# Kernel optimization log

Measured on AMD Instinct MI355X. Metric: run time of the kernel, lower is better.

Reference implementation:

```python
import jax, jax.numpy as jnp
import numpy as np

T, B, DIM, N = 2048, 16, 1024, 64
INIT_BETA_BIAS = 2.0
EPS = 1e-6


def setup_inputs() -> dict:
    key = jax.random.key(0)
    ks = jax.random.split(key, 6)
    xavier = np.sqrt(2.0 / (N + DIM)).astype(np.float32)
    return {
        "x": jax.random.normal(ks[0], (T, B, DIM), dtype=jnp.float32),
        "S0": jnp.zeros((B, N, N), dtype=jnp.float32),
        "W_k": jax.random.normal(ks[1], (N, DIM), dtype=jnp.float32) * xavier,
        "W_v": jax.random.normal(ks[2], (N, DIM), dtype=jnp.float32) * xavier,
        "W_q": jax.random.normal(ks[3], (N, DIM), dtype=jnp.float32) * xavier,
        "W_beta": jax.random.normal(ks[4], (N, DIM), dtype=jnp.float32) * xavier,
        "b_beta": jnp.full((N,), INIT_BETA_BIAS, dtype=jnp.float32),
    }


def reference(x, S0, W_k, W_v, W_q, W_beta, b_beta):
    # Batched projections: [T, B, dim] @ [dim, n] -> [T, B, n]
    k_all = jnp.einsum("tbd,nd->tbn", x, W_k)
    v_all = jnp.einsum("tbd,nd->tbn", x, W_v)
    q_all = jnp.einsum("tbd,nd->tbn", x, W_q)
    g_all = jax.nn.sigmoid(jnp.einsum("tbd,nd->tbn", x, W_beta) + b_beta)

    def step(S, inp):
        k, v, q, g = inp  # each [B, n]
        k_norm = k / (jnp.linalg.norm(k, axis=-1, keepdims=True) + EPS)
        retrieved = jnp.einsum("bij,bj->bi", S, k_norm)
        delta = v - retrieved
        S_new = g[:, :, None] * S + delta[:, :, None] * k_norm[:, None, :]
        Sq = jnp.einsum("bij,bj->bi", S_new, q)
        out = Sq * jax.nn.silu(Sq)  # self-gated output
        return S_new, out

    S_final, output = jax.lax.scan(step, S0, (k_all, v_all, q_all, g_all))
    return output, S_final
```

## Files before the change

### kernel.cpp

```cpp
#include <hip/hip_runtime.h>
#include <math.h>

#define T_STEPS 2048
#define BATCH   16
#define DIM     1024
#define NSTATE  64
#define NFIELD  256
#define PROJ_TSTRIDE (BATCH * NFIELD)
static constexpr float EPS = 1e-6f;

#define AS1 __attribute__((address_space(1)))
#define AS3 __attribute__((address_space(3)))

typedef _Float16 f16x8 __attribute__((ext_vector_type(8)));
typedef _Float16 f16x4 __attribute__((ext_vector_type(4)));
typedef float    f32x4 __attribute__((ext_vector_type(4)));

template <int CTRL>
__device__ __forceinline__ float dpp_add(float x) {
    int yi = __builtin_amdgcn_update_dpp(0, __float_as_int(x), CTRL, 0xF, 0xF, true);
    return x + __int_as_float(yi);
}
__device__ __forceinline__ float reduce16(float x) {
    x = dpp_add<0x121>(x);
    x = dpp_add<0x122>(x);
    x = dpp_add<0x124>(x);
    x = dpp_add<0x128>(x);
    return x;
}
__device__ __forceinline__ void reduce16x2(float& x, float& y) {
    x = dpp_add<0x121>(x); y = dpp_add<0x121>(y);
    x = dpp_add<0x122>(x); y = dpp_add<0x122>(y);
    x = dpp_add<0x124>(x); y = dpp_add<0x124>(y);
    x = dpp_add<0x128>(x); y = dpp_add<0x128>(y);
}
__device__ __forceinline__ float dotp(const float4& u, const float4& w) {
    float t0 = u.x * w.x; t0 = fmaf(u.y, w.y, t0);
    float t1 = u.z * w.z; t1 = fmaf(u.w, w.w, t1);
    return t0 + t1;
}
__device__ __forceinline__ float dot4r(const float4& u, const float4& w) {
    return reduce16(dotp(u, w));
}


#define PBM   128
#define KSTEP 64
#define NKS   (DIM / KSTEP)

__global__ __launch_bounds__(256) void prep_w16(
    const float* __restrict__ Wk, const float* __restrict__ Wv,
    const float* __restrict__ Wq, const float* __restrict__ Wb,
    _Float16* __restrict__ W16)
{
    const int flat = blockIdx.x * 256 + threadIdx.x;
    const int lane = flat & 63;
    const int st   = (flat >> 6) & 31;
    const int ks   = flat >> 11;
    const int cg = st & 15, kc2 = st >> 4;
    const int col = cg * 16 + (lane & 15);
    const int field = col >> 6, wrow = col & 63;
    const float* Wf = (field == 0 ? Wk : field == 1 ? Wv : field == 2 ? Wq : Wb);
    const float* src = Wf + (size_t)wrow * DIM + ks * 64 + kc2 * 32 + (lane >> 4) * 8;
    const float4 a = *(const float4*)(src);
    const float4 b = *(const float4*)(src + 4);
    f16x8 r;
    r[0] = (_Float16)a.x; r[1] = (_Float16)a.y; r[2] = (_Float16)a.z; r[3] = (_Float16)a.w;
    r[4] = (_Float16)b.x; r[5] = (_Float16)b.y; r[6] = (_Float16)b.z; r[7] = (_Float16)b.w;
    *(f16x8*)(W16 + (size_t)flat * 8) = r;
}

__global__ __launch_bounds__(512, 1) void proj_mfma(
    const float* __restrict__ x, const _Float16* __restrict__ W16,
    const float* __restrict__ bb, float* __restrict__ proj)
{
    __shared__ _Float16 Asub[2][16][64][8];
    __shared__ _Float16 Bsub[2][32][64][8];

    const int tid = threadIdx.x;
    const int w = tid >> 6, wl = tid & 63;
    const int wm = w >> 2, wn = w & 3;
    const int l15 = wl & 15, lr = wl >> 4;
    const size_t mbase = (size_t)blockIdx.x * PBM;

    _Float16* const abase = &Asub[0][0][0][0];
    _Float16* const bbase = &Bsub[0][0][0][0];

    const float* asrc[4];
    int aoff[4];
    #pragma unroll
    for (int it = 0; it < 4; ++it) {
        const int fid = it * 512 + tid;
        const int row = fid >> 4, kq = (fid & 15) * 4;
        asrc[it] = x + (mbase + row) * (size_t)DIM + kq;
        aoff[it] = ((kq >> 5) * 8 + (row >> 4)) * 512
                 + ((row & 15) + ((kq >> 3) & 3) * 16) * 8
                 + (kq & 7);
    }
    const _Float16* bsrc[4];
    int boff[4];
    #pragma unroll
    for (int m = 0; m < 4; ++m) {
        const int st = w * 4 + m;
        bsrc[m] = W16 + ((size_t)st * 64 + wl) * 8;
        boff[m] = st * 512;
    }

    auto stageB = [&](int ks, int buf) {
        #pragma unroll
        for (int m = 0; m < 4; ++m) {
            const _Float16* g = bsrc[m] + (size_t)ks * 16384;
            void* lp = (char*)bbase + (size_t)(buf * 16384 + boff[m]) * 2;
            __builtin_amdgcn_global_load_lds((const AS1 void*)g, (AS3 void*)lp, 16, 0, 0);
        }
    };

    float4 h0[4], h1[4];
    auto loadA = [&](int ks, float4* h) {
        #pragma unroll
        for (int it = 0; it < 4; ++it)
            h[it] = *(const float4*)(asrc[it] + ks * KSTEP);
    };
    auto writeA = [&](const float4* h, int buf) {
        #pragma unroll
        for (int it = 0; it < 4; ++it) {
            f16x4 v;
            v[0] = (_Float16)h[it].x; v[1] = (_Float16)h[it].y;
            v[2] = (_Float16)h[it].z; v[3] = (_Float16)h[it].w;
            *(f16x4*)(abase + buf * 8192 + aoff[it]) = v;
        }
    };

    f32x4 acc[4][4] = {};

    loadA(0, h0);
    stageB(0, 0);
    loadA(1, h1);
    writeA(h0, 0);
    __syncthreads();

    #pragma unroll
    for (int ks = 0; ks < NKS; ++ks) {
        const int buf = ks & 1;
        if (ks + 1 < NKS) stageB(ks + 1, buf ^ 1);
        if (ks + 2 < NKS) loadA(ks + 2, (ks & 1) ? h1 : h0);

        #pragma unroll
        for (int kc = 0; kc < 2; ++kc) {
            f16x8 af[4], bf[4];
            #pragma unroll
            for (int mf = 0; mf < 4; ++mf)
                af[mf] = *(const f16x8*)&Asub[buf][kc * 8 + wm * 4 + mf][wl][0];
            #pragma unroll
            for (int nf = 0; nf < 4; ++nf)
                bf[nf] = *(const f16x8*)&Bsub[buf][kc * 16 + wn * 4 + nf][wl][0];
            #pragma unroll
            for (int mf = 0; mf < 4; ++mf)
                #pragma unroll
                for (int nf = 0; nf < 4; ++nf)
                    acc[mf][nf] = __builtin_amdgcn_mfma_f32_16x16x32_f16(
                        af[mf], bf[nf], acc[mf][nf], 0, 0, 0);
        }

        if (ks + 1 < NKS) writeA((ks & 1) ? h0 : h1, buf ^ 1);
        __syncthreads();
    }

    if (wn == 0) {
        #pragma unroll
        for (int mf = 0; mf < 4; ++mf) {
            f32x4 s = acc[mf][0] * acc[mf][0];
            #pragma unroll
            for (int nf = 1; nf < 4; ++nf) s += acc[mf][nf] * acc[mf][nf];
            #pragma unroll
            for (int r = 0; r < 4; ++r) {
                float t = s[r];
                t += __shfl_xor(t, 1); t += __shfl_xor(t, 2);
                t += __shfl_xor(t, 4); t += __shfl_xor(t, 8);
                const float sc = 1.f / (sqrtf(t) + EPS);
                #pragma unroll
                for (int nf = 0; nf < 4; ++nf) acc[mf][nf][r] *= sc;
            }
        }
    }
    if (wn == 3) {
        #pragma unroll
        for (int nf = 0; nf < 4; ++nf) {
            const float bv = bb[nf * 16 + l15];
            #pragma unroll
            for (int mf = 0; mf < 4; ++mf)
                #pragma unroll
                for (int r = 0; r < 4; ++r)
                    acc[mf][nf][r] = 1.f / (1.f + __expf(-(acc[mf][nf][r] + bv)));
        }
    }

    #pragma unroll
    for (int mf = 0; mf < 4; ++mf)
        #pragma unroll
        for (int r = 0; r < 4; ++r) {
            float* dst = proj + (mbase + wm * 64 + mf * 16 + lr * 4 + r) * NFIELD
                              + wn * 64 + l15;
            dst[0]  = acc[mf][0][r];
            dst[16] = acc[mf][1][r];
            dst[32] = acc[mf][2][r];
            dst[48] = acc[mf][3][r];
        }
}

#define KAP_T 2112

__global__ __launch_bounds__(256) void kappa_kernel(
    const float* __restrict__ proj, float* __restrict__ kap2)
{
    const int tid = threadIdx.x;
    const int gid = blockIdx.x * 16 + (tid >> 4);
    const int l   = tid & 15;
    const int t = gid >> 4, b = gid & 15;
    if (t >= T_STEPS) {
        if (l == 0) *(float2*)(kap2 + (size_t)gid * 2) = make_float2(0.f, 0.f);
        return;
    }
    const float* base = proj + ((size_t)t * BATCH + b) * NFIELD;
    const float4 k0 = *(const float4*)(base + 4 * l);
    const float4 q0 = *(const float4*)(base + 128 + 4 * l);
    float cp = 0.f;
    float cq = dotp(k0, q0);
    if (t + 1 < T_STEPS) {
        const float4 k1 = *(const float4*)(base + PROJ_TSTRIDE + 4 * l);
        cp = dotp(k0, k1);
    }
    reduce16x2(cp, cq);
    if (l == 0) *(float2*)(kap2 + (size_t)gid * 2) = make_float2(cp, cq);
}


#define CH 32
#define NCHUNK (T_STEPS / CH)

__global__ __launch_bounds__(128, 1) void scan_kernel(
    const float* __restrict__ proj,
    const float* __restrict__ kap2,
    const float* __restrict__ S0,
    float* __restrict__ out,
    float* __restrict__ Sfin)
{
    __shared__ float KQ[2][CH][128];
    __shared__ float VG[2][CH][16];
    __shared__ float KP2[2][CH][2];

    const int tid = threadIdx.x;
    const int l   = tid & 15;
    const int grp = tid >> 4;
    const int b   = blockIdx.x >> 3;
    const int i0  = (blockIdx.x & 7) * 8;
    const int i   = i0 + grp;
    const int c0  = l * 4;

    const size_t srow = ((size_t)(b * 64 + i)) * 64 + c0;
    float4 S = *(const float4*)(S0 + srow);

    const float* pb = proj + (size_t)b * NFIELD;
    const int wid = tid >> 6, wl = tid & 63;

    const int l31  = wl & 31;
    const int kq_f = l31 * 4 + ((l31 >= 16) ? 64 : 0);
    const int kq_s = wl >> 5;
    const int idx  = wl & 15;
    const int vg_f = (idx & 1) ? (192 + i0 + (idx >> 1)) : (64 + i0 + (idx >> 1));
    const int vg_s = wl >> 4;

    auto stage = [&](int c, int nb) {
        const float* cbase = pb + (size_t)c * CH * PROJ_TSTRIDE;
        #pragma unroll
        for (int m = 0; m < 8; ++m) {
            const int n = wid * 8 + m;
            const float* g = cbase + (size_t)(2 * n + kq_s) * PROJ_TSTRIDE + kq_f;
            void* lp = (char*)&KQ[nb][0][0] + n * 1024;
            __builtin_amdgcn_global_load_lds((const AS1 void*)g, (AS3 void*)lp, 16, 0, 0);
        }
        #pragma unroll
        for (int m = 0; m < 4; ++m) {
            const int p = wid * 4 + m;
            const float* g = cbase + (size_t)(4 * p + vg_s) * PROJ_TSTRIDE + vg_f;
            void* lp = (char*)&VG[nb][0][0] + p * 256;
            __builtin_amdgcn_global_load_lds((const AS1 void*)g, (AS3 void*)lp, 4, 0, 0);
        }
        if (wid == 0) {
            const float* g = kap2 + ((size_t)(c * CH + (wl >> 1)) * BATCH + b) * 2
                           + (wl & 1);
            void* lp = (char*)&KP2[nb][0][0];
            __builtin_amdgcn_global_load_lds((const AS1 void*)g, (AS3 void*)lp, 4, 0, 0);
        }
    };

    float4 kn_s[4], q_s[4];
    float2 vg_s4[4], kk_s[4];
    auto ldslot = [&](int cb2, int s, int j) {
        kn_s[j]  = *(const float4*)(&KQ[cb2][s][c0]);
        q_s[j]   = *(const float4*)(&KQ[cb2][s][64 + c0]);
        vg_s4[j] = *(const float2*)(&VG[cb2][s][2 * grp]);
        kk_s[j]  = *(const float2*)(&KP2[cb2][s][0]);
    };

    stage(0, 0);
    __syncthreads();

    float a, cqr, cpr;
    auto prime = [&](int nb) {
        #pragma unroll
        for (int j = 0; j < 4; ++j) ldslot(nb, j, j);
        float aP  = dotp(S, kn_s[0]);
        float cqP = dotp(S, q_s[0]);
        float cpP = dotp(S, kn_s[1]);
        reduce16x2(aP, cqP);
        cpP = reduce16(cpP);
        a = aP; cqr = cqP; cpr = cpP;
    };
    prime(0);

    float osel = 0.f;

    for (int c = 0; c < NCHUNK; ++c) {
        const int cb = c & 1;
        const bool more = (c + 1 < NCHUNK);
        if (more) stage(c + 1, cb ^ 1);

        #pragma unroll
        for (int s = 0; s < CH; ++s) {
            const int j = s & 3;

            const float4 kn = kn_s[j];
            const float  v = vg_s4[j].x, g = vg_s4[j].y;
            const float2 kk = kk_s[j];

            const float d  = v - a;
            const float sq = fmaf(d, kk.y, g * cqr);
            const float an = fmaf(d, kk.x, g * cpr);

            S.x = fmaf(d, kn.x, g * S.x);
            S.y = fmaf(d, kn.y, g * S.y);
            S.z = fmaf(d, kn.z, g * S.z);
            S.w = fmaf(d, kn.w, g * S.w);

            if (s + 4 < CH) ldslot(cb, s + 4, j);

            if (s + 2 < CH) {
                float cqP = dotp(S, q_s[(s + 1) & 3]);
                float cpP = dotp(S, kn_s[(s + 2) & 3]);
                reduce16x2(cpP, cqP);
                cpr = cpP; cqr = cqP;
            } else if (s + 1 < CH) {
                cqr = reduce16(dotp(S, q_s[(s + 1) & 3]));
            }
            a = an;

            osel = ((s & 15) == l) ? sq : osel;
            if ((s & 15) == 15) {
                const float y = osel * osel / (1.f + __expf(-osel));
                const int tbase = c * CH + (s - 15);
                out[((size_t)(tbase + l) * BATCH + b) * 64 + i] = y;
            }
        }

        if (more) {
            __syncthreads();
            prime(cb ^ 1);
        }
    }

    *(float4*)(Sfin + srow) = S;
}

extern "C" void kernel_launch(void* const* d_in, const int* in_sizes, int n_in,
                              void* d_out, int out_size, void* d_ws, size_t ws_size,
                              hipStream_t stream) {
    const float* x  = (const float*)d_in[0];
    const float* S0 = (const float*)d_in[1];
    const float* Wk = (const float*)d_in[2];
    const float* Wv = (const float*)d_in[3];
    const float* Wq = (const float*)d_in[4];
    const float* Wb = (const float*)d_in[5];
    const float* bb = (const float*)d_in[6];

    float* out  = (float*)d_out;
    float* Sfin = out + (size_t)T_STEPS * BATCH * NSTATE;

    float*    proj = (float*)d_ws;
    float*    kap2 = proj + (size_t)T_STEPS * BATCH * NFIELD;
    _Float16* W16  = (_Float16*)(kap2 + (size_t)KAP_T * BATCH * 2);

    prep_w16<<<128, 256, 0, stream>>>(Wk, Wv, Wq, Wb, W16);
    proj_mfma<<<(T_STEPS * BATCH) / PBM, 512, 0, stream>>>(x, W16, bb, proj);
    kappa_kernel<<<KAP_T, 256, 0, stream>>>(proj, kap2);
    scan_kernel<<<(BATCH * NSTATE) / 8, 128, 0, stream>>>(proj, kap2, S0, out, Sfin);
}
```

Before: 416.3 us.

## Split scan state rows across 32 lanes with 256-thread blocks

The scan kernel now gives each state row to 32 lanes holding two columns each, where before 16 lanes held four columns each. Blocks grow from 128 to 256 threads, and the dot-product reductions gain an extra ds_swizzle xor-16 step. The goal is to halve the serial per-thread arithmetic on the recurrence's critical path and use more lanes per CU. In exchange, each reduction is longer and includes an LDS-path swizzle, output writes happen once per 32 steps, and chunk priming moves to the top of the loop ahead of the next chunk's staging.

```diff
diff --git a/kernel.cpp b/kernel.cpp
--- a/kernel.cpp
+++ b/kernel.cpp
@@ -21,12 +21,28 @@
     int yi = __builtin_amdgcn_update_dpp(0, __float_as_int(x), CTRL, 0xF, 0xF, true);
     return x + __int_as_float(yi);
 }
-__device__ __forceinline__ float reduce16(float x) {
-    x = dpp_add<0x121>(x);
-    x = dpp_add<0x122>(x);
-    x = dpp_add<0x124>(x);
-    x = dpp_add<0x128>(x);
-    return x;
+__device__ __forceinline__ float xor16_add(float x) {
+    int y = __builtin_amdgcn_ds_swizzle(__float_as_int(x), 0x401F);
+    return x + __int_as_float(y);
+}
+__device__ __forceinline__ float reduce32(float x) {
+    x = dpp_add<0x121>(x); x = dpp_add<0x122>(x);
+    x = dpp_add<0x124>(x); x = dpp_add<0x128>(x);
+    return xor16_add(x);
+}
+__device__ __forceinline__ void reduce32x2(float& x, float& y) {
+    x = dpp_add<0x121>(x); y = dpp_add<0x121>(y);
+    x = dpp_add<0x122>(x); y = dpp_add<0x122>(y);
+    x = dpp_add<0x124>(x); y = dpp_add<0x124>(y);
+    x = dpp_add<0x128>(x); y = dpp_add<0x128>(y);
+    x = xor16_add(x);      y = xor16_add(y);
+}
+__device__ __forceinline__ void reduce32x3(float& x, float& y, float& z) {
+    x = dpp_add<0x121>(x); y = dpp_add<0x121>(y); z = dpp_add<0x121>(z);
+    x = dpp_add<0x122>(x); y = dpp_add<0x122>(y); z = dpp_add<0x122>(z);
+    x = dpp_add<0x124>(x); y = dpp_add<0x124>(y); z = dpp_add<0x124>(z);
+    x = dpp_add<0x128>(x); y = dpp_add<0x128>(y); z = dpp_add<0x128>(z);
+    x = xor16_add(x);      y = xor16_add(y);      z = xor16_add(z);
 }
 __device__ __forceinline__ void reduce16x2(float& x, float& y) {
     x = dpp_add<0x121>(x); y = dpp_add<0x121>(y);
@@ -39,8 +55,8 @@
     float t1 = u.z * w.z; t1 = fmaf(u.w, w.w, t1);
     return t0 + t1;
 }
-__device__ __forceinline__ float dot4r(const float4& u, const float4& w) {
-    return reduce16(dotp(u, w));
+__device__ __forceinline__ float dotp2(const float2& u, const float2& w) {
+    return fmaf(u.y, w.y, u.x * w.x);
 }
 
 
@@ -238,7 +254,7 @@
 #define CH 32
 #define NCHUNK (T_STEPS / CH)
 
-__global__ __launch_bounds__(128, 1) void scan_kernel(
+__global__ __launch_bounds__(256, 1) void scan_kernel(
     const float* __restrict__ proj,
     const float* __restrict__ kap2,
     const float* __restrict__ S0,
@@ -249,44 +265,45 @@
     __shared__ float VG[2][CH][16];
     __shared__ float KP2[2][CH][2];
 
-    const int tid = threadIdx.x;
-    const int l   = tid & 15;
-    const int grp = tid >> 4;
-    const int b   = blockIdx.x >> 3;
-    const int i0  = (blockIdx.x & 7) * 8;
-    const int i   = i0 + grp;
-    const int c0  = l * 4;
+    const int tid  = threadIdx.x;
+    const int w    = tid >> 6;
+    const int wl   = tid & 63;
+    const int half = wl >> 5;
+    const int jl   = wl & 31;
+    const int b    = blockIdx.x >> 3;
+    const int i0   = (blockIdx.x & 7) * 8;
+    const int i    = i0 + 2 * w + half;
+    const int c0   = 2 * jl;
 
     const size_t srow = ((size_t)(b * 64 + i)) * 64 + c0;
-    float4 S = *(const float4*)(S0 + srow);
+    float2 S = *(const float2*)(S0 + srow);
 
     const float* pb = proj + (size_t)b * NFIELD;
-    const int wid = tid >> 6, wl = tid & 63;
 
     const int l31  = wl & 31;
     const int kq_f = l31 * 4 + ((l31 >= 16) ? 64 : 0);
     const int kq_s = wl >> 5;
     const int idx  = wl & 15;
     const int vg_f = (idx & 1) ? (192 + i0 + (idx >> 1)) : (64 + i0 + (idx >> 1));
-    const int vg_s = wl >> 4;
+    const int vg_sl = wl >> 4;
 
     auto stage = [&](int c, int nb) {
         const float* cbase = pb + (size_t)c * CH * PROJ_TSTRIDE;
         #pragma unroll
-        for (int m = 0; m < 8; ++m) {
-            const int n = wid * 8 + m;
+        for (int m = 0; m < 4; ++m) {
+            const int n = w * 4 + m;
             const float* g = cbase + (size_t)(2 * n + kq_s) * PROJ_TSTRIDE + kq_f;
             void* lp = (char*)&KQ[nb][0][0] + n * 1024;
             __builtin_amdgcn_global_load_lds((const AS1 void*)g, (AS3 void*)lp, 16, 0, 0);
         }
         #pragma unroll
-        for (int m = 0; m < 4; ++m) {
-            const int p = wid * 4 + m;
-            const float* g = cbase + (size_t)(4 * p + vg_s) * PROJ_TSTRIDE + vg_f;
+        for (int m = 0; m < 2; ++m) {
+            const int p = w * 2 + m;
+            const float* g = cbase + (size_t)(4 * p + vg_sl) * PROJ_TSTRIDE + vg_f;
             void* lp = (char*)&VG[nb][0][0] + p * 256;
             __builtin_amdgcn_global_load_lds((const AS1 void*)g, (AS3 void*)lp, 4, 0, 0);
         }
-        if (wid == 0) {
+        if (w == 0) {
             const float* g = kap2 + ((size_t)(c * CH + (wl >> 1)) * BATCH + b) * 2
                            + (wl & 1);
             void* lp = (char*)&KP2[nb][0][0];
@@ -294,35 +311,38 @@
         }
     };
 
-    float4 kn_s[4], q_s[4];
-    float2 vg_s4[4], kk_s[4];
-    auto ldslot = [&](int cb2, int s, int j) {
-        kn_s[j]  = *(const float4*)(&KQ[cb2][s][c0]);
-        q_s[j]   = *(const float4*)(&KQ[cb2][s][64 + c0]);
-        vg_s4[j] = *(const float2*)(&VG[cb2][s][2 * grp]);
-        kk_s[j]  = *(const float2*)(&KP2[cb2][s][0]);
-    };
+    float2 kn_r[4], q_r[4], vg_r[4], kk_r[4];
+    const int vgo = 2 * (2 * w + half);
 
     stage(0, 0);
     __syncthreads();
 
     float a, cqr, cpr;
-    auto prime = [&](int nb) {
-        #pragma unroll
-        for (int j = 0; j < 4; ++j) ldslot(nb, j, j);
-        float aP  = dotp(S, kn_s[0]);
-        float cqP = dotp(S, q_s[0]);
-        float cpP = dotp(S, kn_s[1]);
-        reduce16x2(aP, cqP);
-        cpP = reduce16(cpP);
-        a = aP; cqr = cqP; cpr = cpP;
-    };
-    prime(0);
-
     float osel = 0.f;
 
     for (int c = 0; c < NCHUNK; ++c) {
         const int cb = c & 1;
+        const float (*KQc)[128] = KQ[cb];
+        const float (*VGc)[16]  = VG[cb];
+        const float (*KPc)[2]   = KP2[cb];
+
+        auto ldslot = [&](int s, int j) {
+            kn_r[j] = *(const float2*)(&KQc[s][c0]);
+            q_r [j] = *(const float2*)(&KQc[s][64 + c0]);
+            vg_r[j] = *(const float2*)(&VGc[s][vgo]);
+            kk_r[j] = *(const float2*)(&KPc[s][0]);
+        };
+
+        #pragma unroll
+        for (int j = 0; j < 4; ++j) ldslot(j, j);
+        {
+            float aP  = dotp2(S, kn_r[0]);
+            float cqP = dotp2(S, q_r[0]);
+            float cpP = dotp2(S, kn_r[1]);
+            reduce32x3(aP, cqP, cpP);
+            a = aP; cqr = cqP; cpr = cpP;
+        }
+
         const bool more = (c + 1 < NCHUNK);
         if (more) stage(c + 1, cb ^ 1);
 
@@ -330,9 +350,9 @@
         for (int s = 0; s < CH; ++s) {
             const int j = s & 3;
 
-            const float4 kn = kn_s[j];
-            const float  v = vg_s4[j].x, g = vg_s4[j].y;
-            const float2 kk = kk_s[j];
+            const float2 kn = kn_r[j];
+            const float  v = vg_r[j].x, g = vg_r[j].y;
+            const float2 kk = kk_r[j];
 
             const float d  = v - a;
             const float sq = fmaf(d, kk.y, g * cqr);
@@ -340,36 +360,30 @@
 
             S.x = fmaf(d, kn.x, g * S.x);
             S.y = fmaf(d, kn.y, g * S.y);
-            S.z = fmaf(d, kn.z, g * S.z);
-            S.w = fmaf(d, kn.w, g * S.w);
-
-            if (s + 4 < CH) ldslot(cb, s + 4, j);
+
+            if (s + 4 < CH) ldslot(s + 4, j);
 
             if (s + 2 < CH) {
-                float cqP = dotp(S, q_s[(s + 1) & 3]);
-                float cpP = dotp(S, kn_s[(s + 2) & 3]);
-                reduce16x2(cpP, cqP);
+                float cqP = dotp2(S, q_r[(s + 1) & 3]);
+                float cpP = dotp2(S, kn_r[(s + 2) & 3]);
+                reduce32x2(cpP, cqP);
                 cpr = cpP; cqr = cqP;
             } else if (s + 1 < CH) {
-                cqr = reduce16(dotp(S, q_s[(s + 1) & 3]));
+                cqr = reduce32(dotp2(S, q_r[(s + 1) & 3]));
             }
             a = an;
 
-            osel = ((s & 15) == l) ? sq : osel;
-            if ((s & 15) == 15) {
+            osel = (s == jl) ? sq : osel;
+            if (s == CH - 1) {
                 const float y = osel * osel / (1.f + __expf(-osel));
-                const int tbase = c * CH + (s - 15);
-                out[((size_t)(tbase + l) * BATCH + b) * 64 + i] = y;
+                out[((size_t)(c * CH + jl) * BATCH + b) * 64 + i] = y;
             }
         }
 
-        if (more) {
-            __syncthreads();
-            prime(cb ^ 1);
-        }
-    }
-
-    *(float4*)(Sfin + srow) = S;
+        if (more) __syncthreads();
+    }
+
+    *(float2*)(Sfin + srow) = S;
 }
 
 extern "C" void kernel_launch(void* const* d_in, const int* in_sizes, int n_in,
@@ -393,5 +407,5 @@
     prep_w16<<<128, 256, 0, stream>>>(Wk, Wv, Wq, Wb, W16);
     proj_mfma<<<(T_STEPS * BATCH) / PBM, 512, 0, stream>>>(x, W16, bb, proj);
     kappa_kernel<<<KAP_T, 256, 0, stream>>>(proj, kap2);
-    scan_kernel<<<(BATCH * NSTATE) / 8, 128, 0, stream>>>(proj, kap2, S0, out, Sfin);
-}
+    scan_kernel<<<(BATCH * NSTATE) / 8, 256, 0, stream>>>(proj, kap2, S0, out, Sfin);
+}
```

After: 445.7 us. +7.1%, slower.
